# Performance work log

Measured on AMD Instinct MI355X. Metric: run time of the kernel, lower is better.

Reference implementation:

```python
import jax, jax.numpy as jnp
import numpy as np

N_NODES = 50000
N_EDGES = 800000
D_IN, D_HID, D_ENC = 256, 128, 64


def setup_inputs() -> dict:
    key = jax.random.key(0)
    ks = jax.random.split(key, 8)
    x = jax.random.normal(ks[0], (N_NODES, D_IN), dtype=jnp.float32)
    edge_index = jax.random.randint(ks[1], (2, N_EDGES), 0, N_NODES, dtype=jnp.int64)
    # GCNConv params: lin weight (no bias) + separate bias, stored as [in, out]
    W1 = jax.random.normal(ks[2], (D_IN, D_HID), dtype=jnp.float32) * (1.0 / np.sqrt(D_IN))
    b1 = jnp.zeros((D_HID,), dtype=jnp.float32)
    W2 = jax.random.normal(ks[3], (D_HID, D_ENC), dtype=jnp.float32) * (1.0 / np.sqrt(D_HID))
    b2 = jnp.zeros((D_ENC,), dtype=jnp.float32)
    Wfc = jax.random.normal(ks[4], (D_ENC, 1), dtype=jnp.float32) * (1.0 / np.sqrt(D_ENC))
    bfc = jnp.zeros((1,), dtype=jnp.float32)
    return {"x": x, "edge_index": edge_index, "W1": W1, "b1": b1,
            "W2": W2, "b2": b2, "Wfc": Wfc, "bfc": bfc}


def gcn_conv(x, W, b, row, col, norm, n_nodes):
    """PyG GCNConv (normalize=True): D^-1/2 (A+I) D^-1/2 X W + b."""
    h = x @ W                                   # [N, out]
    msg = h[row] * norm[:, None]                # [E+N, out] gather + scale
    out = jax.ops.segment_sum(msg, col, num_segments=n_nodes)  # scatter-add
    return out + b


def gcn_norm(edge_index, n_nodes, dtype):
    loop = jnp.arange(n_nodes, dtype=edge_index.dtype)
    row = jnp.concatenate([edge_index[0], loop])  # sources
    col = jnp.concatenate([edge_index[1], loop])  # targets
    deg = jax.ops.segment_sum(jnp.ones_like(col, dtype=dtype), col,
                              num_segments=n_nodes)
    dinv = jnp.where(deg > 0, jax.lax.rsqrt(jnp.maximum(deg, 1e-12)), 0.0)
    norm = dinv[row] * dinv[col]
    return row, col, norm


def reference(x, edge_index, W1, b1, W2, b2, Wfc, bfc):
    n = x.shape[0]
    row, col, norm = gcn_norm(edge_index, n, x.dtype)
    h = gcn_conv(x, W1, b1, row, col, norm, n)
    h = jax.nn.relu(h)
    # dropout p=0 / eval mode: identity
    h = gcn_conv(h, W2, b2, row, col, norm, n)
    out = jax.nn.sigmoid(h @ Wfc + bfc)          # [N, 1]
    return out
```

## Files before the change

kernel.cpp:

```cpp
#include <hip/hip_runtime.h>
#include <hip/hip_bf16.h>
#include <cmath>

#define N_NODES 50000
#define N_EDGES 800000
#define D_IN 256
#define D_HID 128
#define D_ENC 64
#define NBUK 128
#define BSH 9
#define BMSK 511
#define BCAP 16384
#define PB_EPT 16

typedef short short8 __attribute__((ext_vector_type(8)));
typedef float floatx4 __attribute__((ext_vector_type(4)));
typedef float floatx8 __attribute__((ext_vector_type(8)));
typedef unsigned short ushort8v __attribute__((ext_vector_type(8)));

static __device__ __forceinline__ unsigned short f2bf(float f) {
    unsigned int u = __float_as_uint(f);
    unsigned int r = (u + 0x7FFFu + ((u >> 16) & 1u)) >> 16;
    return (unsigned short)r;
}
static __device__ __forceinline__ float bf2f(unsigned short u) {
    return __uint_as_float(((unsigned int)u) << 16);
}
static __device__ __forceinline__ floatx8 bf2f8(ushort8v u) {
    floatx8 f;
#pragma unroll
    for (int j = 0; j < 8; ++j) f[j] = bf2f(u[j]);
    return f;
}

static __device__ __forceinline__ void wswz(const float* __restrict__ W,
                                            unsigned short* __restrict__ Wsw,
                                            int t, int K, int N) {
    int KS = K / 32;
    int lane = t & 63;
    int ks   = (t >> 6) % KS;
    int ct   = (t >> 6) / KS;
    int m = lane & 15, quad = lane >> 4;
    int kbase = ks * 32 + quad * 8;
    int col   = ct * 16 + m;
#pragma unroll
    for (int j = 0; j < 8; ++j)
        Wsw[t * 8 + j] = f2bf(W[(size_t)(kbase + j) * N + col]);
}

__global__ __launch_bounds__(256) void part_k(const int* __restrict__ rows,
                                              const int* __restrict__ cols,
                                              int* __restrict__ bcur,
                                              unsigned int* __restrict__ brecs,
                                              const float* __restrict__ W1,
                                              const float* __restrict__ W2,
                                              unsigned short* __restrict__ Wsw1,
                                              unsigned short* __restrict__ Wsw2) {
    __shared__ unsigned int recs[256 * PB_EPT];
    __shared__ int h[NBUK], ex[NBUK], gbase[NBUK];
    int tid = threadIdx.x;
    int t = blockIdx.x * 256 + tid;
    if (t < 4096) wswz(W1, Wsw1, t, D_IN, D_HID);
    else if (t < 5120) wswz(W2, Wsw2, t - 4096, D_HID, D_ENC);

    if (tid < NBUK) h[tid] = 0;
    __syncthreads();
    int e0 = blockIdx.x * (256 * PB_EPT);
    unsigned int myrec[PB_EPT];
    int myb[PB_EPT];
#pragma unroll
    for (int j = 0; j < PB_EPT; ++j) {
        int e = e0 + j * 256 + tid;
        if (e < N_EDGES) {
            int s = rows[e], d = cols[e];
            myrec[j] = ((unsigned int)s << 16) | (unsigned int)d;
            myb[j] = d >> BSH;
            atomicAdd(&h[myb[j]], 1);
        } else myb[j] = -1;
    }
    __syncthreads();
    if (tid < NBUK) {
        int c = h[tid];
        gbase[tid] = tid * BCAP + (c ? atomicAdd(&bcur[tid], c) : 0);
        ex[tid] = c;
    }
    __syncthreads();
    for (int off = 1; off < NBUK; off <<= 1) {
        int v = 0;
        if (tid < NBUK && tid >= off) v = ex[tid - off];
        __syncthreads();
        if (tid < NBUK) ex[tid] += v;
        __syncthreads();
    }
    if (tid < NBUK) { ex[tid] -= h[tid]; h[tid] = 0; }
    __syncthreads();
#pragma unroll
    for (int j = 0; j < PB_EPT; ++j) {
        if (myb[j] >= 0) {
            int p = ex[myb[j]] + atomicAdd(&h[myb[j]], 1);
            recs[p] = myrec[j];
        }
    }
    __syncthreads();
    int w = tid >> 6, lane = tid & 63;
    for (int b = w; b < NBUK; b += 4) {
        int start = ex[b], cnt = h[b], gb = gbase[b];
        int lim = (b + 1) * BCAP;
        for (int i = lane; i < cnt; i += 64) {
            int gp = gb + i;
            if (gp < lim) brecs[gp] = recs[start + i];
        }
    }
}

__global__ __launch_bounds__(512) void bucket_csr_k(const unsigned int* __restrict__ brecs,
                                                    const int* __restrict__ bcur,
                                                    int* __restrict__ rowptr,
                                                    int* __restrict__ rowcnt,
                                                    unsigned short* __restrict__ srcs,
                                                    float* __restrict__ dinv) {
    __shared__ int s[512];
    __shared__ int cur[512];
    __shared__ unsigned short sl[BCAP];
    int b = blockIdx.x;
    int cb = bcur[b]; if (cb > BCAP) cb = BCAP;
    int ebeg = b * BCAP, eend = ebeg + cb;
    int tid = threadIdx.x;
    s[tid] = 0;
    __syncthreads();
    for (int e = ebeg + tid; e < eend; e += 512)
        atomicAdd(&s[brecs[e] & BMSK], 1);
    __syncthreads();
    int v = s[tid];
    for (int off = 1; off < 512; off <<= 1) {
        int t = (tid >= off) ? s[tid - off] : 0;
        __syncthreads();
        s[tid] += t;
        __syncthreads();
    }
    int excl = s[tid] - v;
    cur[tid] = excl;
    int node = (b << BSH) + tid;
    if (node < N_NODES) {
        rowptr[node] = ebeg + excl;
        rowcnt[node] = v;
        dinv[node] = rsqrtf((float)(v + 1));
    }
    __syncthreads();
    for (int e = ebeg + tid; e < eend; e += 512) {
        unsigned int rec = brecs[e];
        int p = atomicAdd(&cur[rec & BMSK], 1);
        sl[p] = (unsigned short)(rec >> 16);
    }
    __syncthreads();
    int nw = (cb + 1) >> 1;
    unsigned int* s32 = (unsigned int*)(srcs + ebeg);
    const unsigned int* l32 = (const unsigned int*)sl;
    for (int t = tid; t < nw; t += 512) s32[t] = l32[t];
}

template<int K, int N, bool IN_BF16>
__global__ __launch_bounds__(256) void gemm_mfma_k(const void* __restrict__ Xv,
                                                   const unsigned short* __restrict__ Wsw,
                                                   const float* __restrict__ dinv,
                                                   unsigned short* __restrict__ H, int n) {
    constexpr int KS = K / 32, CT = N / 16, KP = K + 8;
    __shared__ unsigned short As[64 * KP];
    int row0 = blockIdx.x * 64;
    if (IN_BF16) {
        const ushort8v* X8 = (const ushort8v*)Xv;
        constexpr int NF8 = 64 * (K / 8);
        for (int idx = threadIdx.x; idx < NF8; idx += 256) {
            int r = idx / (K / 8), c8 = idx % (K / 8);
            int gr = row0 + r;
            ushort8v v = (gr < n) ? X8[(size_t)gr * (K / 8) + c8] : (ushort8v)0;
            *(ushort8v*)&As[r * KP + c8 * 8] = v;
        }
    } else {
        const float4* X4 = (const float4*)Xv;
        constexpr int NF4 = 64 * (K / 4);
        for (int idx = threadIdx.x; idx < NF4; idx += 256) {
            int r = idx / (K / 4), c4 = idx % (K / 4);
            int gr = row0 + r;
            float4 v = (gr < n) ? X4[(size_t)gr * (K / 4) + c4] : float4{0, 0, 0, 0};
            __hip_bfloat162 p0 = __float22bfloat162_rn(float2{v.x, v.y});
            __hip_bfloat162 p1 = __float22bfloat162_rn(float2{v.z, v.w});
            uint2 u; u.x = *(unsigned int*)&p0; u.y = *(unsigned int*)&p1;
            *(uint2*)&As[r * KP + c4 * 4] = u;
        }
    }
    __syncthreads();

    int w    = threadIdx.x >> 6;
    int lane = threadIdx.x & 63;
    int m    = lane & 15;
    int quad = lane >> 4;

    floatx4 acc[CT];
#pragma unroll
    for (int ct = 0; ct < CT; ++ct)
#pragma unroll
        for (int i = 0; i < 4; ++i) acc[ct][i] = 0.0f;

#pragma unroll
    for (int ks = 0; ks < KS; ++ks) {
        short8 af = *(const short8*)&As[(w * 16 + m) * KP + ks * 32 + quad * 8];
#pragma unroll
        for (int ct = 0; ct < CT; ++ct) {
            short8 bf = *(const short8*)&Wsw[(size_t)((ct * KS + ks) * 64 + lane) * 8];
            acc[ct] = __builtin_amdgcn_mfma_f32_16x16x32_bf16(af, bf, acc[ct], 0, 0, 0);
        }
    }

    int rbase = row0 + w * 16 + quad * 4;
    float dv[4];
#pragma unroll
    for (int reg = 0; reg < 4; ++reg) {
        int r = rbase + reg;
        dv[reg] = (r < n) ? dinv[r] : 0.0f;
    }
#pragma unroll
    for (int ct = 0; ct < CT; ++ct)
#pragma unroll
        for (int reg = 0; reg < 4; ++reg) {
            int r = rbase + reg;
            if (r < n) H[(size_t)r * N + ct * 16 + m] = f2bf(acc[ct][reg] * dv[reg]);
        }
}

#define GATHER_LOOP(SP, STRIDE, D)                                             \
    {                                                                          \
        const auto* sp_ = (SP);                                                \
        int i = 0;                                                             \
        for (; i + 8 <= cnt; i += 8) {                                         \
            int s0 = sp_[i],     s1 = sp_[i + 1], s2 = sp_[i + 2], s3 = sp_[i + 3]; \
            int s4 = sp_[i + 4], s5 = sp_[i + 5], s6 = sp_[i + 6], s7 = sp_[i + 7]; \
            ushort8v v0 = hs[(size_t)s0 * STRIDE + D], v1 = hs[(size_t)s1 * STRIDE + D]; \
            ushort8v v2 = hs[(size_t)s2 * STRIDE + D], v3 = hs[(size_t)s3 * STRIDE + D]; \
            ushort8v v4 = hs[(size_t)s4 * STRIDE + D], v5 = hs[(size_t)s5 * STRIDE + D]; \
            ushort8v v6 = hs[(size_t)s6 * STRIDE + D], v7 = hs[(size_t)s7 * STRIDE + D]; \
            a0 += bf2f8(v0); a1 += bf2f8(v1); a2 += bf2f8(v2); a3 += bf2f8(v3); \
            a0 += bf2f8(v4); a1 += bf2f8(v5); a2 += bf2f8(v6); a3 += bf2f8(v7); \
        }                                                                      \
        if (i + 4 <= cnt) {                                                    \
            int s0 = sp_[i], s1 = sp_[i + 1], s2 = sp_[i + 2], s3 = sp_[i + 3]; \
            a0 += bf2f8(hs[(size_t)s0 * STRIDE + D]);                          \
            a1 += bf2f8(hs[(size_t)s1 * STRIDE + D]);                          \
            a2 += bf2f8(hs[(size_t)s2 * STRIDE + D]);                          \
            a3 += bf2f8(hs[(size_t)s3 * STRIDE + D]);                          \
            i += 4;                                                            \
        }                                                                      \
        for (; i < cnt; ++i)                                                   \
            a0 += bf2f8(hs[(size_t)sp_[i] * STRIDE + D]);                      \
    }

__global__ __launch_bounds__(256) void g1g2_k(const ushort8v* __restrict__ hs,
                                              const int* __restrict__ rowptr,
                                              const int* __restrict__ rowcnt,
                                              const unsigned short* __restrict__ srcs,
                                              const float* __restrict__ dinv,
                                              const float4* __restrict__ b1_4,
                                              const unsigned short* __restrict__ Wsw2,
                                              unsigned short* __restrict__ h2) {
    constexpr int KP = D_HID + 8;
    __shared__ unsigned short As[16 * KP];
    __shared__ unsigned short sidx[1024];
    __shared__ int sb2[2];
    int tid = threadIdx.x;
    int nodeb = blockIdx.x * 16;
    int ln = tid >> 4;
    int d8 = tid & 15;
    int node = nodeb + ln;
    int beg = rowptr[node];
    int cnt = rowcnt[node];
    if (tid == 0)   sb2[0] = beg;
    if (tid == 240) sb2[1] = beg + cnt;
    ushort8v selfv = hs[(size_t)node * 16 + d8];
    float di = dinv[node];
    __syncthreads();
    int base = sb2[0], total = sb2[1] - base;
    for (int t = tid; t < total && t < 1024; t += 256) sidx[t] = srcs[base + t];
    __syncthreads();

    floatx8 a0 = {0,0,0,0,0,0,0,0}, a1 = a0, a2 = a0, a3 = a0;
    if (total <= 1024) {
        GATHER_LOOP(sidx + (beg - base), 16, d8)
    } else {
        GATHER_LOOP(srcs + beg, 16, d8)
    }
    floatx8 acc = a0 + a1 + a2 + a3 + bf2f8(selfv);
    float4 bA = b1_4[d8 * 2], bB = b1_4[d8 * 2 + 1];
    ushort8v r;
    r[0] = f2bf(fmaxf(di * acc[0] + bA.x, 0.0f));
    r[1] = f2bf(fmaxf(di * acc[1] + bA.y, 0.0f));
    r[2] = f2bf(fmaxf(di * acc[2] + bA.z, 0.0f));
    r[3] = f2bf(fmaxf(di * acc[3] + bA.w, 0.0f));
    r[4] = f2bf(fmaxf(di * acc[4] + bB.x, 0.0f));
    r[5] = f2bf(fmaxf(di * acc[5] + bB.y, 0.0f));
    r[6] = f2bf(fmaxf(di * acc[6] + bB.z, 0.0f));
    r[7] = f2bf(fmaxf(di * acc[7] + bB.w, 0.0f));
    *(ushort8v*)&As[ln * KP + d8 * 8] = r;
    __syncthreads();

    constexpr int KS = D_HID / 32;
    int w    = tid >> 6;
    int lane = tid & 63;
    int m = lane & 15, quad = lane >> 4;
    floatx4 acc2 = {0, 0, 0, 0};
#pragma unroll
    for (int ks = 0; ks < KS; ++ks) {
        short8 af = *(const short8*)&As[m * KP + ks * 32 + quad * 8];
        short8 bf = *(const short8*)&Wsw2[(size_t)((w * KS + ks) * 64 + lane) * 8];
        acc2 = __builtin_amdgcn_mfma_f32_16x16x32_bf16(af, bf, acc2, 0, 0, 0);
    }
#pragma unroll
    for (int reg = 0; reg < 4; ++reg) {
        int nn = nodeb + quad * 4 + reg;
        h2[(size_t)nn * D_ENC + w * 16 + m] = f2bf(acc2[reg] * dinv[nn]);
    }
}

__global__ __launch_bounds__(256) void gather2_k(const ushort8v* __restrict__ hs, const int* __restrict__ rowptr,
                          const int* __restrict__ rowcnt, const unsigned short* __restrict__ srcs,
                          const float* __restrict__ dinv,
                          const float4* __restrict__ b4, const float4* __restrict__ Wfc4,
                          const float* __restrict__ bfc, float* __restrict__ out) {
    __shared__ unsigned short sidx[1536];
    __shared__ int sb2[2];
    int tid = threadIdx.x;
    int node = blockIdx.x * 32 + (tid >> 3);
    int d8   = tid & 7;
    bool valid = node < N_NODES;
    int cn  = valid ? node : N_NODES - 1;
    int beg = rowptr[cn];
    int rc  = rowcnt[cn];
    int cnt = valid ? rc : 0;
    if (tid == 0)   sb2[0] = beg;
    if (tid == 248) sb2[1] = beg + rc;
    ushort8v selfv = hs[(size_t)cn * 8 + d8];
    float di = dinv[cn];
    __syncthreads();
    int base = sb2[0], total = sb2[1] - base;
    for (int t = tid; t < total && t < 1536; t += 256) sidx[t] = srcs[base + t];
    __syncthreads();

    floatx8 a0 = {0,0,0,0,0,0,0,0}, a1 = a0, a2 = a0, a3 = a0;
    if (total <= 1536) {
        GATHER_LOOP(sidx + (beg - base), 8, d8)
    } else {
        GATHER_LOOP(srcs + beg, 8, d8)
    }
    floatx8 acc = a0 + a1 + a2 + a3 + bf2f8(selfv);
    float4 bA = b4[d8 * 2], bB = b4[d8 * 2 + 1];
    float4 wA = Wfc4[d8 * 2], wB = Wfc4[d8 * 2 + 1];
    float p = (di * acc[0] + bA.x) * wA.x + (di * acc[1] + bA.y) * wA.y
            + (di * acc[2] + bA.z) * wA.z + (di * acc[3] + bA.w) * wA.w
            + (di * acc[4] + bB.x) * wB.x + (di * acc[5] + bB.y) * wB.y
            + (di * acc[6] + bB.z) * wB.z + (di * acc[7] + bB.w) * wB.w;
#pragma unroll
    for (int off = 4; off; off >>= 1) p += __shfl_down(p, off, 8);
    if (valid && d8 == 0) out[node] = 1.0f / (1.0f + expf(-(p + bfc[0])));
}

extern "C" void kernel_launch(void* const* d_in, const int* in_sizes, int n_in,
                              void* d_out, int out_size, void* d_ws, size_t ws_size,
                              hipStream_t stream) {
    const float* x   = (const float*)d_in[0];
    const int*   ei  = (const int*)d_in[1];
    const float* W1  = (const float*)d_in[2];
    const float* b1  = (const float*)d_in[3];
    const float* W2  = (const float*)d_in[4];
    const float* b2  = (const float*)d_in[5];
    const float* Wfc = (const float*)d_in[6];
    const float* bfc = (const float*)d_in[7];
    float* out = (float*)d_out;

    const int* rows = ei;
    const int* cols = ei + N_EDGES;

    float* ws     = (float*)d_ws;
    float* dinv   = ws;
    int*   rowptr = (int*)(ws + 50048);
    int*   rowcnt = rowptr + 50048;
    int*   bcur   = rowcnt + 50048;
    unsigned int* brecs = (unsigned int*)(bcur + 128);
    unsigned short* srcs = (unsigned short*)(brecs + NBUK * BCAP);
    unsigned short* h1 = srcs + (size_t)NBUK * BCAP;
    unsigned short* h2 = h1 + (size_t)N_NODES * D_HID;
    unsigned short* Wsw1 = h2 + (size_t)N_NODES * D_ENC;
    unsigned short* Wsw2 = Wsw1 + (size_t)D_IN * D_HID;

    hipMemsetAsync(bcur, 0, NBUK * sizeof(int), stream);
    part_k<<<(N_EDGES + 256 * PB_EPT - 1) / (256 * PB_EPT), 256, 0, stream>>>(
        rows, cols, bcur, brecs, W1, W2, Wsw1, Wsw2);
    bucket_csr_k<<<(N_NODES + 511) / 512, 512, 0, stream>>>(brecs, bcur, rowptr, rowcnt, srcs, dinv);

    gemm_mfma_k<D_IN, D_HID, false><<<(N_NODES + 63) / 64, 256, 0, stream>>>(x, Wsw1, dinv, h1, N_NODES);

    g1g2_k<<<N_NODES / 16, 256, 0, stream>>>((const ushort8v*)h1, rowptr, rowcnt, srcs, dinv,
                                             (const float4*)b1, Wsw2, h2);

    gather2_k<<<(N_NODES + 31) / 32, 256, 0, stream>>>((const ushort8v*)h2, rowptr, rowcnt, srcs, dinv,
                                                       (const float4*)b2, (const float4*)Wfc,
                                                       bfc, out);
}
```

Before: 190.4 us.

## Fold W2 and Wfc into one vector and aggregate scalars in layer two

```diff
diff --git a/kernel.cpp b/kernel.cpp
--- a/kernel.cpp
+++ b/kernel.cpp
@@ -54,14 +54,27 @@
                                               unsigned int* __restrict__ brecs,
                                               const float* __restrict__ W1,
                                               const float* __restrict__ W2,
+                                              const float* __restrict__ b2,
+                                              const float* __restrict__ Wfc,
                                               unsigned short* __restrict__ Wsw1,
-                                              unsigned short* __restrict__ Wsw2) {
+                                              float* __restrict__ w2fc,
+                                              float* __restrict__ b2fc) {
     __shared__ unsigned int recs[256 * PB_EPT];
     __shared__ int h[NBUK], ex[NBUK], gbase[NBUK];
     int tid = threadIdx.x;
     int t = blockIdx.x * 256 + tid;
     if (t < 4096) wswz(W1, Wsw1, t, D_IN, D_HID);
-    else if (t < 5120) wswz(W2, Wsw2, t - 4096, D_HID, D_ENC);
+    else if (t < 4224) {
+        int c = t - 4096;
+        float s = 0.0f;
+#pragma unroll 8
+        for (int j = 0; j < D_ENC; ++j) s += W2[c * D_ENC + j] * Wfc[j];
+        w2fc[c] = s;
+    } else if (t == 4224) {
+        float s = 0.0f;
+        for (int j = 0; j < D_ENC; ++j) s += b2[j] * Wfc[j];
+        b2fc[0] = s;
+    }
 
     if (tid < NBUK) h[tid] = 0;
     __syncthreads();
@@ -254,16 +267,14 @@
             a0 += bf2f8(hs[(size_t)sp_[i] * STRIDE + D]);                      \
     }
 
-__global__ __launch_bounds__(256) void g1g2_k(const ushort8v* __restrict__ hs,
-                                              const int* __restrict__ rowptr,
-                                              const int* __restrict__ rowcnt,
-                                              const unsigned short* __restrict__ srcs,
-                                              const float* __restrict__ dinv,
-                                              const float4* __restrict__ b1_4,
-                                              const unsigned short* __restrict__ Wsw2,
-                                              unsigned short* __restrict__ h2) {
-    constexpr int KP = D_HID + 8;
-    __shared__ unsigned short As[16 * KP];
+__global__ __launch_bounds__(256) void g1z_k(const ushort8v* __restrict__ hs,
+                                             const int* __restrict__ rowptr,
+                                             const int* __restrict__ rowcnt,
+                                             const unsigned short* __restrict__ srcs,
+                                             const float* __restrict__ dinv,
+                                             const float4* __restrict__ b1_4,
+                                             const float4* __restrict__ w2fc4,
+                                             float* __restrict__ z) {
     __shared__ unsigned short sidx[1024];
     __shared__ int sb2[2];
     int tid = threadIdx.x;
@@ -289,77 +300,43 @@
         GATHER_LOOP(srcs + beg, 16, d8)
     }
     floatx8 acc = a0 + a1 + a2 + a3 + bf2f8(selfv);
-    float4 bA = b1_4[d8 * 2], bB = b1_4[d8 * 2 + 1];
-    ushort8v r;
-    r[0] = f2bf(fmaxf(di * acc[0] + bA.x, 0.0f));
-    r[1] = f2bf(fmaxf(di * acc[1] + bA.y, 0.0f));
-    r[2] = f2bf(fmaxf(di * acc[2] + bA.z, 0.0f));
-    r[3] = f2bf(fmaxf(di * acc[3] + bA.w, 0.0f));
-    r[4] = f2bf(fmaxf(di * acc[4] + bB.x, 0.0f));
-    r[5] = f2bf(fmaxf(di * acc[5] + bB.y, 0.0f));
-    r[6] = f2bf(fmaxf(di * acc[6] + bB.z, 0.0f));
-    r[7] = f2bf(fmaxf(di * acc[7] + bB.w, 0.0f));
-    *(ushort8v*)&As[ln * KP + d8 * 8] = r;
-    __syncthreads();
-
-    constexpr int KS = D_HID / 32;
-    int w    = tid >> 6;
-    int lane = tid & 63;
-    int m = lane & 15, quad = lane >> 4;
-    floatx4 acc2 = {0, 0, 0, 0};
-#pragma unroll
-    for (int ks = 0; ks < KS; ++ks) {
-        short8 af = *(const short8*)&As[m * KP + ks * 32 + quad * 8];
-        short8 bf = *(const short8*)&Wsw2[(size_t)((w * KS + ks) * 64 + lane) * 8];
-        acc2 = __builtin_amdgcn_mfma_f32_16x16x32_bf16(af, bf, acc2, 0, 0, 0);
-    }
-#pragma unroll
-    for (int reg = 0; reg < 4; ++reg) {
-        int nn = nodeb + quad * 4 + reg;
-        h2[(size_t)nn * D_ENC + w * 16 + m] = f2bf(acc2[reg] * dinv[nn]);
-    }
-}
-
-__global__ __launch_bounds__(256) void gather2_k(const ushort8v* __restrict__ hs, const int* __restrict__ rowptr,
-                          const int* __restrict__ rowcnt, const unsigned short* __restrict__ srcs,
-                          const float* __restrict__ dinv,
-                          const float4* __restrict__ b4, const float4* __restrict__ Wfc4,
-                          const float* __restrict__ bfc, float* __restrict__ out) {
-    __shared__ unsigned short sidx[1536];
-    __shared__ int sb2[2];
-    int tid = threadIdx.x;
-    int node = blockIdx.x * 32 + (tid >> 3);
-    int d8   = tid & 7;
-    bool valid = node < N_NODES;
-    int cn  = valid ? node : N_NODES - 1;
-    int beg = rowptr[cn];
-    int rc  = rowcnt[cn];
-    int cnt = valid ? rc : 0;
-    if (tid == 0)   sb2[0] = beg;
-    if (tid == 248) sb2[1] = beg + rc;
-    ushort8v selfv = hs[(size_t)cn * 8 + d8];
-    float di = dinv[cn];
-    __syncthreads();
-    int base = sb2[0], total = sb2[1] - base;
-    for (int t = tid; t < total && t < 1536; t += 256) sidx[t] = srcs[base + t];
-    __syncthreads();
-
-    floatx8 a0 = {0,0,0,0,0,0,0,0}, a1 = a0, a2 = a0, a3 = a0;
-    if (total <= 1536) {
-        GATHER_LOOP(sidx + (beg - base), 8, d8)
-    } else {
-        GATHER_LOOP(srcs + beg, 8, d8)
-    }
-    floatx8 acc = a0 + a1 + a2 + a3 + bf2f8(selfv);
-    float4 bA = b4[d8 * 2], bB = b4[d8 * 2 + 1];
-    float4 wA = Wfc4[d8 * 2], wB = Wfc4[d8 * 2 + 1];
-    float p = (di * acc[0] + bA.x) * wA.x + (di * acc[1] + bA.y) * wA.y
-            + (di * acc[2] + bA.z) * wA.z + (di * acc[3] + bA.w) * wA.w
-            + (di * acc[4] + bB.x) * wB.x + (di * acc[5] + bB.y) * wB.y
-            + (di * acc[6] + bB.z) * wB.z + (di * acc[7] + bB.w) * wB.w;
-#pragma unroll
-    for (int off = 4; off; off >>= 1) p += __shfl_down(p, off, 8);
-    if (valid && d8 == 0) out[node] = 1.0f / (1.0f + expf(-(p + bfc[0])));
+    float4 bA = b1_4[d8 * 2],  bB = b1_4[d8 * 2 + 1];
+    float4 wA = w2fc4[d8 * 2], wB = w2fc4[d8 * 2 + 1];
+    float s = fmaxf(di * acc[0] + bA.x, 0.0f) * wA.x
+            + fmaxf(di * acc[1] + bA.y, 0.0f) * wA.y
+            + fmaxf(di * acc[2] + bA.z, 0.0f) * wA.z
+            + fmaxf(di * acc[3] + bA.w, 0.0f) * wA.w
+            + fmaxf(di * acc[4] + bB.x, 0.0f) * wB.x
+            + fmaxf(di * acc[5] + bB.y, 0.0f) * wB.y
+            + fmaxf(di * acc[6] + bB.z, 0.0f) * wB.z
+            + fmaxf(di * acc[7] + bB.w, 0.0f) * wB.w;
+#pragma unroll
+    for (int off = 8; off; off >>= 1) s += __shfl_xor(s, off, 16);
+    if (d8 == 0) z[node] = di * s;
+}
+
+__global__ __launch_bounds__(256) void gatherz_k(const float* __restrict__ z,
+                                                 const int* __restrict__ rowptr,
+                                                 const int* __restrict__ rowcnt,
+                                                 const unsigned short* __restrict__ srcs,
+                                                 const float* __restrict__ dinv,
+                                                 const float* __restrict__ b2fc,
+                                                 const float* __restrict__ bfc,
+                                                 float* __restrict__ out) {
+    int v = blockIdx.x * 256 + threadIdx.x;
+    if (v >= N_NODES) return;
+    int beg = rowptr[v], cnt = rowcnt[v];
+    float s0 = z[v], s1 = 0.0f, s2 = 0.0f, s3 = 0.0f;
+    int i = beg, end = beg + cnt;
+    for (; i + 4 <= end; i += 4) {
+        s0 += z[srcs[i]];
+        s1 += z[srcs[i + 1]];
+        s2 += z[srcs[i + 2]];
+        s3 += z[srcs[i + 3]];
+    }
+    for (; i < end; ++i) s0 += z[srcs[i]];
+    float p = dinv[v] * (s0 + s1 + s2 + s3) + b2fc[0] + bfc[0];
+    out[v] = 1.0f / (1.0f + expf(-p));
 }
 
 extern "C" void kernel_launch(void* const* d_in, const int* in_sizes, int n_in,
@@ -386,21 +363,21 @@
     unsigned int* brecs = (unsigned int*)(bcur + 128);
     unsigned short* srcs = (unsigned short*)(brecs + NBUK * BCAP);
     unsigned short* h1 = srcs + (size_t)NBUK * BCAP;
-    unsigned short* h2 = h1 + (size_t)N_NODES * D_HID;
-    unsigned short* Wsw1 = h2 + (size_t)N_NODES * D_ENC;
-    unsigned short* Wsw2 = Wsw1 + (size_t)D_IN * D_HID;
+    unsigned short* Wsw1 = h1 + (size_t)N_NODES * D_HID;
+    float* z    = (float*)(Wsw1 + (size_t)D_IN * D_HID);
+    float* w2fc = z + 50000;
+    float* b2fc = w2fc + 128;
 
     hipMemsetAsync(bcur, 0, NBUK * sizeof(int), stream);
     part_k<<<(N_EDGES + 256 * PB_EPT - 1) / (256 * PB_EPT), 256, 0, stream>>>(
-        rows, cols, bcur, brecs, W1, W2, Wsw1, Wsw2);
+        rows, cols, bcur, brecs, W1, W2, b2, Wfc, Wsw1, w2fc, b2fc);
     bucket_csr_k<<<(N_NODES + 511) / 512, 512, 0, stream>>>(brecs, bcur, rowptr, rowcnt, srcs, dinv);
 
     gemm_mfma_k<D_IN, D_HID, false><<<(N_NODES + 63) / 64, 256, 0, stream>>>(x, Wsw1, dinv, h1, N_NODES);
 
-    g1g2_k<<<N_NODES / 16, 256, 0, stream>>>((const ushort8v*)h1, rowptr, rowcnt, srcs, dinv,
-                                             (const float4*)b1, Wsw2, h2);
-
-    gather2_k<<<(N_NODES + 31) / 32, 256, 0, stream>>>((const ushort8v*)h2, rowptr, rowcnt, srcs, dinv,
-                                                       (const float4*)b2, (const float4*)Wfc,
-                                                       bfc, out);
-}
+    g1z_k<<<N_NODES / 16, 256, 0, stream>>>((const ushort8v*)h1, rowptr, rowcnt, srcs, dinv,
+                                            (const float4*)b1, (const float4*)w2fc, z);
+
+    gatherz_k<<<(N_NODES + 255) / 256, 256, 0, stream>>>(z, rowptr, rowcnt, srcs, dinv,
+                                                         b2fc, bfc, out);
+}
```

Result: faster. 179.3 us (-5.8%).
